# Kernel optimization log

Hardware: AMD Instinct MI355X
Metric: run time of the kernel (lower is better)

## Reference

```python
import jax, jax.numpy as jnp
import numpy as np

NUM_HEADS = 16
EPS = 1e-5
CHUNK = 128  # chunk length for the chunked recurrent-state scan


def _linear_attention(x, Wq, Wk, Wv, Wo, bo):
    B, T, E = x.shape
    H = NUM_HEADS
    d = E // H

    def proj(W):
        # nn.Linear(bias=False): y = x @ W.T ; split heads -> (B,H,T,d)
        return (x @ W.T).reshape(B, T, H, d).transpose(0, 2, 1, 3)

    phi_q = jax.nn.elu(proj(Wq)) + 1.0
    phi_k = jax.nn.elu(proj(Wk)) + 1.0
    V = proj(Wv)

    nC = T // CHUNK
    # (nC, B, H, C, d) so lax.scan iterates over chunks of time
    def to_chunks(a):
        return a.reshape(B, H, nC, CHUNK, d).transpose(2, 0, 1, 3, 4)

    qc, kc, vc = to_chunks(phi_q), to_chunks(phi_k), to_chunks(V)
    mask = jnp.tril(jnp.ones((CHUNK, CHUNK), x.dtype))  # causal incl. diagonal

    S0 = jnp.zeros((B, H, d, d), x.dtype)  # running sum of k v^T
    z0 = jnp.zeros((B, H, d), x.dtype)     # running sum of phi_k

    def step(carry, inp):
        S, z = carry
        q, k, v = inp  # (B,H,C,d)
        A = jnp.einsum('bhid,bhjd->bhij', q, k) * mask
        num = jnp.einsum('bhij,bhjd->bhid', A, v) + jnp.einsum('bhid,bhde->bhie', q, S)
        den = jnp.sum(A, axis=-1) + jnp.einsum('bhid,bhd->bhi', q, z) + EPS
        out = num / den[..., None]
        S = S + jnp.einsum('bhjd,bhje->bhde', k, v)
        z = z + jnp.sum(k, axis=2)
        return (S, z), out

    _, outs = jax.lax.scan(step, (S0, z0), (qc, kc, vc))  # (nC,B,H,C,d)
    out = outs.transpose(1, 2, 0, 3, 4).reshape(B, H, T, d)
    out = out.transpose(0, 2, 1, 3).reshape(B, T, E)
    # out_proj (dropout p=0 / eval -> identity)
    return out @ Wo.T + bo


def setup_inputs() -> dict:
    key = jax.random.key(0)
    ks = jax.random.split(key, 6)
    B, T, E = 2, 2048, 1024
    s = 1.0 / np.sqrt(E)
    return {
        'x': jax.random.normal(ks[0], (B, T, E), jnp.float32),
        'Wq': jax.random.normal(ks[1], (E, E), jnp.float32) * s,
        'Wk': jax.random.normal(ks[2], (E, E), jnp.float32) * s,
        'Wv': jax.random.normal(ks[3], (E, E), jnp.float32) * s,
        'Wo': jax.random.normal(ks[4], (E, E), jnp.float32) * s,
        'bo': jnp.zeros((E,), jnp.float32),
    }


def reference(x, Wq, Wk, Wv, Wo, bo):
    return _linear_attention(x, Wq, Wk, Wv, Wo, bo)
```

## Files before the change

### kernel.cpp

```cpp
#include <hip/hip_runtime.h>
#include <hip/hip_bf16.h>
#include <stdint.h>

typedef __attribute__((ext_vector_type(4)))  float  floatx4;
typedef __attribute__((ext_vector_type(8)))  short  short8;
typedef __attribute__((ext_vector_type(8)))  unsigned short ushortx8;
typedef __attribute__((ext_vector_type(4)))  unsigned short ushortx4;

#define B_  2
#define T_  2048
#define E_  1024
#define H_  16
#define D_  64
#define C_  128
#define NC_ 16
#define M_  4096
#define EPS_ 1e-5f

__device__ __forceinline__ unsigned short f2b(float f) {
    union { float f; unsigned int u; } v; v.f = f;
    unsigned int r = v.u + 0x7fffu + ((v.u >> 16) & 1u);
    return (unsigned short)(r >> 16);
}
__device__ __forceinline__ float b2f(unsigned short b) {
    union { unsigned int u; float f; } v; v.u = ((unsigned int)b) << 16;
    return v.f;
}

__device__ __forceinline__ int stage_seg(int i) { return (i & 3) ^ ((i >> 3) & 3); }
__device__ __forceinline__ int frag_slot(int lane) {
    int m = lane & 15, q = lane >> 4;
    return m * 4 + (q ^ ((m >> 1) & 3));
}

__global__ __launch_bounds__(256) void convert_all(const float* __restrict__ x,
                                                   const float* __restrict__ Wq,
                                                   const float* __restrict__ Wk,
                                                   const float* __restrict__ Wv,
                                                   const float* __restrict__ Wo,
                                                   unsigned short* __restrict__ dst) {
    int i = (blockIdx.x * 256 + threadIdx.x) * 4;
    const float* s; int off;
    if (i < M_ * E_) { s = x; off = i; }
    else {
        int j = i - M_ * E_;
        int which = j >> 20;
        s = (which == 0) ? Wq : (which == 1) ? Wk : (which == 2) ? Wv : Wo;
        off = j & ((1 << 20) - 1);
    }
    float4 f = *(const float4*)(s + off);
    ushortx4 o;
    o[0] = f2b(f.x); o[1] = f2b(f.y); o[2] = f2b(f.z); o[3] = f2b(f.w);
    *(ushortx4*)(dst + i) = o;
}

__global__ __launch_bounds__(512) void gemm_qkv(const unsigned short* __restrict__ A,
                                                const unsigned short* __restrict__ Bm,
                                                unsigned short* __restrict__ Cb) {
    const int N = 3 * E_, K = E_;
    __shared__ __align__(16) unsigned short smem[57344];
    unsigned short* at0 = smem;
    unsigned short* bt0 = smem + 16384;
    unsigned short* at1 = smem + 28672;
    unsigned short* bt1 = smem + 45056;
    int tid = threadIdx.x;
    int wave = tid >> 6, lane = tid & 63;
    int wr = wave >> 2, wc = wave & 3;
    int m = lane & 15, q = lane >> 4;
    int srow = lane >> 2, sseg = stage_seg(lane);
    int fs = frag_slot(lane);
    int row0 = blockIdx.y * 256, col0 = blockIdx.x * 192;
    floatx4 acc[8][3];
    for (int i = 0; i < 8; i++) for (int j = 0; j < 3; j++) acc[i][j] = floatx4{0.f, 0.f, 0.f, 0.f};

    auto stageA = [&](unsigned short* at, int k0) {
        for (int p = 0; p < 4; p++) {
            int t = p * 8 + wave;
            const unsigned short* ga = A + (size_t)(row0 + (t & 15) * 16 + srow) * K + k0 + (t >> 4) * 32 + sseg * 8;
            __builtin_amdgcn_global_load_lds((const __attribute__((address_space(1))) unsigned int*)ga,
                (__attribute__((address_space(3))) unsigned int*)(at + t * 512), 16, 0, 0);
        }
    };
    auto stageB = [&](unsigned short* bt, int k0) {
        for (int p = 0; p < 3; p++) {
            int u = p * 8 + wave;
            int kh = u / 12, rb = u - kh * 12;
            const unsigned short* gb = Bm + (size_t)(col0 + rb * 16 + srow) * K + k0 + kh * 32 + sseg * 8;
            __builtin_amdgcn_global_load_lds((const __attribute__((address_space(1))) unsigned int*)gb,
                (__attribute__((address_space(3))) unsigned int*)(bt + u * 512), 16, 0, 0);
        }
    };
    short8 af[8], bf[3];
    auto frags = [&](const unsigned short* at, const unsigned short* bt, int kh) {
        for (int mi = 0; mi < 8; mi++) af[mi] = *(const short8*)(at + (kh * 16 + wr * 8 + mi) * 512 + fs * 8);
        for (int ni = 0; ni < 3; ni++) bf[ni] = *(const short8*)(bt + (kh * 12 + wc * 3 + ni) * 512 + fs * 8);
    };
    auto mfma24 = [&]() {
        __builtin_amdgcn_s_setprio(1);
        for (int mi = 0; mi < 8; mi++)
            for (int ni = 0; ni < 3; ni++)
                acc[mi][ni] = __builtin_amdgcn_mfma_f32_16x16x32_bf16(af[mi], bf[ni], acc[mi][ni], 0, 0, 0);
        __builtin_amdgcn_s_setprio(0);
    };

    stageA(at0, 0); stageB(bt0, 0);
    for (int k0 = 0; k0 < K; k0 += 128) {
        stageA(at1, k0 + 64);
        asm volatile("s_waitcnt vmcnt(4)" ::: "memory");
        __builtin_amdgcn_s_barrier();
        frags(at0, bt0, 0);
        mfma24();
        frags(at0, bt0, 1);
        stageB(bt1, k0 + 64);
        mfma24();
        __builtin_amdgcn_s_barrier();
        if (k0 + 128 < K) {
            stageA(at0, k0 + 128);
            asm volatile("s_waitcnt vmcnt(4)" ::: "memory");
        } else {
            asm volatile("s_waitcnt vmcnt(0)" ::: "memory");
        }
        __builtin_amdgcn_s_barrier();
        frags(at1, bt1, 0);
        mfma24();
        frags(at1, bt1, 1);
        if (k0 + 128 < K) stageB(bt0, k0 + 128);
        mfma24();
        __builtin_amdgcn_s_barrier();
    }

    unsigned short* epi = smem + wave * 1792;
    for (int ch = 0; ch < 4; ch++) {
        if (ch) asm volatile("" ::: "memory");
        for (int mi2 = 0; mi2 < 2; mi2++) {
            int mi = ch * 2 + mi2;
            for (int ni = 0; ni < 3; ni++)
                for (int reg = 0; reg < 4; reg++) {
                    int lr = mi2 * 16 + q * 4 + reg;
                    int colw = col0 + wc * 48 + ni * 16 + m;
                    float v = acc[mi][ni][reg];
                    if (colw < 2 * E_) v = (v > 0.f) ? (v + 1.f) : __expf(v);
                    epi[lr * 56 + ni * 16 + m] = f2b(v);
                }
        }
        asm volatile("" ::: "memory");
        for (int slot = 0; slot < 3; slot++) {
            int s = slot * 64 + lane;
            int lr = s / 6, seg = s - lr * 6;
            const unsigned short* p = epi + lr * 56 + seg * 8;
            ushortx4 lo = *(const ushortx4*)(p);
            ushortx4 hi = *(const ushortx4*)(p + 4);
            ushortx8 val;
            for (int e = 0; e < 4; e++) { val[e] = lo[e]; val[e + 4] = hi[e]; }
            int row = row0 + wr * 128 + ch * 32 + lr;
            int col = col0 + wc * 48 + seg * 8;
            *(ushortx8*)(Cb + (size_t)row * N + col) = val;
        }
    }
}

__global__ __launch_bounds__(256) void gemm_out(const unsigned short* __restrict__ A,
                                                const unsigned short* __restrict__ Bm,
                                                const float* __restrict__ bias,
                                                float* __restrict__ Cf) {
    const int N = E_, K = E_;
    __shared__ __align__(16) unsigned short smem[24576];
    unsigned short* at0 = smem;
    unsigned short* bt0 = smem + 8192;
    unsigned short* at1 = smem + 12288;
    unsigned short* bt1 = smem + 20480;
    int tid = threadIdx.x;
    int wave = tid >> 6, lane = tid & 63;
    int wr = wave >> 1, wc = wave & 1;
    int m = lane & 15, q = lane >> 4;
    int srow = lane >> 2, sseg = stage_seg(lane);
    int fs = frag_slot(lane);
    int row0 = blockIdx.y * 128, col0 = blockIdx.x * 64;
    floatx4 acc[4][2];
    for (int i = 0; i < 4; i++) for (int j = 0; j < 2; j++) acc[i][j] = floatx4{0.f, 0.f, 0.f, 0.f};

    auto stageA = [&](unsigned short* at, int k0) {
        for (int p = 0; p < 4; p++) {
            int t = p * 4 + wave;
            const unsigned short* ga = A + (size_t)(row0 + (t & 7) * 16 + srow) * K + k0 + (t >> 3) * 32 + sseg * 8;
            __builtin_amdgcn_global_load_lds((const __attribute__((address_space(1))) unsigned int*)ga,
                (__attribute__((address_space(3))) unsigned int*)(at + t * 512), 16, 0, 0);
        }
    };
    auto stageB = [&](unsigned short* bt, int k0) {
        for (int p = 0; p < 2; p++) {
            int u = p * 4 + wave;
            const unsigned short* gb = Bm + (size_t)(col0 + (u & 3) * 16 + srow) * K + k0 + (u >> 2) * 32 + sseg * 8;
            __builtin_amdgcn_global_load_lds((const __attribute__((address_space(1))) unsigned int*)gb,
                (__attribute__((address_space(3))) unsigned int*)(bt + u * 512), 16, 0, 0);
        }
    };
    short8 af[4], bf[2];
    auto frags = [&](const unsigned short* at, const unsigned short* bt, int kh) {
        for (int mi = 0; mi < 4; mi++) af[mi] = *(const short8*)(at + (kh * 8 + wr * 4 + mi) * 512 + fs * 8);
        for (int ci = 0; ci < 2; ci++) bf[ci] = *(const short8*)(bt + (kh * 4 + wc * 2 + ci) * 512 + fs * 8);
    };
    auto mfma8 = [&]() {
        __builtin_amdgcn_s_setprio(1);
        for (int mi = 0; mi < 4; mi++)
            for (int ci = 0; ci < 2; ci++)
                acc[mi][ci] = __builtin_amdgcn_mfma_f32_16x16x32_bf16(af[mi], bf[ci], acc[mi][ci], 0, 0, 0);
        __builtin_amdgcn_s_setprio(0);
    };

    stageA(at0, 0); stageB(bt0, 0);
    for (int k0 = 0; k0 < K; k0 += 128) {
        stageA(at1, k0 + 64);
        asm volatile("s_waitcnt vmcnt(4)" ::: "memory");
        __builtin_amdgcn_s_barrier();
        frags(at0, bt0, 0);
        mfma8();
        frags(at0, bt0, 1);
        stageB(bt1, k0 + 64);
        mfma8();
        __builtin_amdgcn_s_barrier();
        if (k0 + 128 < K) {
            stageA(at0, k0 + 128);
            asm volatile("s_waitcnt vmcnt(4)" ::: "memory");
        } else {
            asm volatile("s_waitcnt vmcnt(0)" ::: "memory");
        }
        __builtin_amdgcn_s_barrier();
        frags(at1, bt1, 0);
        mfma8();
        frags(at1, bt1, 1);
        if (k0 + 128 < K) stageB(bt0, k0 + 128);
        mfma8();
        __builtin_amdgcn_s_barrier();
    }

    int qrow = q * 4;
    for (int ci = 0; ci < 2; ci++) {
        int col = col0 + wc * 32 + ci * 16 + m;
        float bv = bias[col];
        for (int mi = 0; mi < 4; mi++)
            for (int r2 = 0; r2 < 4; r2++) {
                int row = row0 + wr * 64 + mi * 16 + qrow + r2;
                Cf[(size_t)row * N + col] = acc[mi][ci][r2] + bv;
            }
    }
}

__global__ __launch_bounds__(256) void chunk_sums(const unsigned short* __restrict__ qkv,
                                                  float* __restrict__ Sc, float* __restrict__ zc) {
    int c = blockIdx.x, h = blockIdx.y, bb = blockIdx.z;
    __shared__ __align__(16) unsigned short Kt[64 * 132];
    __shared__ __align__(16) unsigned short Vt[80 * 132];
    int tid = threadIdx.x;
    int lane = tid & 63, w = tid >> 6;
    size_t rowb = (size_t)bb * T_ + (size_t)c * C_;
    int kcol = E_ + h * D_, vcol = 2 * E_ + h * D_;

    {
        int r4 = (tid >> 3) * 4;
        int seg = (tid & 7) * 8;
        ushortx8 kv[4], vv[4];
        for (int t = 0; t < 4; t++) {
            size_t g = (rowb + r4 + t) * 3072;
            kv[t] = *(const ushortx8*)(qkv + g + kcol + seg);
            vv[t] = *(const ushortx8*)(qkv + g + vcol + seg);
        }
        for (int e = 0; e < 8; e++) {
            ushortx4 ka, va;
            for (int t = 0; t < 4; t++) { ka[t] = kv[t][e]; va[t] = vv[t][e]; }
            *(ushortx4*)(Kt + (seg + e) * 132 + r4) = ka;
            *(ushortx4*)(Vt + (seg + e) * 132 + r4) = va;
        }
    }
    if (tid < 128) Vt[64 * 132 + tid] = 0x3f80;
    __syncthreads();

    floatx4 acc[5];
    for (int ni = 0; ni < 5; ni++) acc[ni] = floatx4{0.f, 0.f, 0.f, 0.f};
    int lm = lane & 15, lk = (lane >> 4) * 8;
    for (int k0 = 0; k0 < 128; k0 += 32) {
        short8 af = *(const short8*)(Kt + (w * 16 + lm) * 132 + k0 + lk);
        for (int ni = 0; ni < 5; ni++) {
            short8 bf = *(const short8*)(Vt + (ni * 16 + lm) * 132 + k0 + lk);
            acc[ni] = __builtin_amdgcn_mfma_f32_16x16x32_bf16(af, bf, acc[ni], 0, 0, 0);
        }
    }
    size_t base = ((size_t)(bb * H_ + h) * NC_ + c) * (size_t)(D_ * D_);
    int r0 = w * 16 + (lane >> 4) * 4;
    for (int ni = 0; ni < 4; ni++)
        for (int reg = 0; reg < 4; reg++)
            Sc[base + (size_t)(r0 + reg) * D_ + ni * 16 + lm] = acc[ni][reg];
    if (lm == 0) {
        size_t zb = ((size_t)(bb * H_ + h) * NC_ + c) * D_;
        for (int reg = 0; reg < 4; reg++) zc[zb + r0 + reg] = acc[4][reg];
    }
}

__global__ __launch_bounds__(256) void attn_kernel(const unsigned short* __restrict__ qkv,
                                                   const float* __restrict__ Sc,
                                                   const float* __restrict__ zc,
                                                   unsigned short* __restrict__ attn) {
    int c = blockIdx.x, h = blockIdx.y, bb = blockIdx.z;
    __shared__ __align__(16) unsigned short ks[128 * 68];
    __shared__ __align__(16) unsigned short vt[64 * 132];
    __shared__ __align__(16) unsigned short ovl[128 * 36];
    __shared__ float zsh[64];
    int tid = threadIdx.x;
    int lane = tid & 63, w = tid >> 6;
    int lm = lane & 15, lq = lane >> 4;
    size_t rowb = (size_t)bb * T_ + (size_t)c * C_;
    int qcol = h * D_, kcol = E_ + h * D_, vcol = 2 * E_ + h * D_;

    for (int s = 0; s < 4; s++) {
        int off = s * 256 + tid;
        int r = off >> 3, seg = (off & 7) * 8;
        ushortx8 k8 = *(const ushortx8*)(qkv + (rowb + r) * 3072 + kcol + seg);
        *(ushortx8*)(ks + r * 68 + seg) = k8;
    }
    {
        int r4 = (tid >> 3) * 4;
        int seg = (tid & 7) * 8;
        ushortx8 vv[4];
        for (int t = 0; t < 4; t++)
            vv[t] = *(const ushortx8*)(qkv + (rowb + r4 + t) * 3072 + vcol + seg);
        for (int e = 0; e < 8; e++) {
            ushortx4 va;
            for (int t = 0; t < 4; t++) va[t] = vv[t][e];
            *(ushortx4*)(vt + (seg + e) * 132 + r4) = va;
        }
    }
    {
        size_t scb = ((size_t)(bb * H_ + h) * NC_) * (size_t)(D_ * D_);
        int p = tid * 16;
        float a[16];
        for (int i = 0; i < 16; i++) a[i] = 0.f;
        for (int j = 0; j < c; j++) {
            const float* Sj = Sc + scb + (size_t)j * (D_ * D_) + p;
            for (int q = 0; q < 16; q += 4) {
                float4 f = *(const float4*)(Sj + q);
                a[q] += f.x; a[q + 1] += f.y; a[q + 2] += f.z; a[q + 3] += f.w;
            }
        }
        for (int i = 0; i < 16; i++) {
            int d = (p + i) >> 6, e = (p + i) & 63;
            ovl[e * 68 + d] = f2b(a[i]);
        }
    }
    if (tid < 64) {
        size_t zb = ((size_t)(bb * H_ + h) * NC_) * D_;
        float zr = 0.f;
        for (int j = 0; j < c; j++) zr += zc[zb + (size_t)j * D_ + tid];
        zsh[tid] = zr;
    }

    short8 aq[2][2];
    for (int mi = 0; mi < 2; mi++)
        for (int kk = 0; kk < 2; kk++)
            aq[mi][kk] = *(const short8*)(qkv + (rowb + w * 32 + mi * 16 + lm) * 3072 + qcol + kk * 32 + lq * 8);
    __syncthreads();

    floatx4 acc[2][4];
    for (int mi = 0; mi < 2; mi++) for (int ni = 0; ni < 4; ni++) acc[mi][ni] = floatx4{0.f, 0.f, 0.f, 0.f};
    for (int kk = 0; kk < 2; kk++)
        for (int ni = 0; ni < 4; ni++) {
            short8 bs = *(const short8*)(ovl + (ni * 16 + lm) * 68 + kk * 32 + lq * 8);
            for (int mi = 0; mi < 2; mi++)
                acc[mi][ni] = __builtin_amdgcn_mfma_f32_16x16x32_bf16(aq[mi][kk], bs, acc[mi][ni], 0, 0, 0);
        }
    float dsum[2][4];
    {
        float4 z4 = *(const float4*)(zsh + lm * 4);
        for (int mi = 0; mi < 2; mi++)
            for (int reg = 0; reg < 4; reg++) {
                int row = w * 32 + mi * 16 + lq * 4 + reg;
                ushortx4 q4 = *(const ushortx4*)(qkv + (rowb + row) * 3072 + qcol + lm * 4);
                dsum[mi][reg] = b2f(q4[0]) * z4.x + b2f(q4[1]) * z4.y + b2f(q4[2]) * z4.z + b2f(q4[3]) * z4.w;
            }
    }
    __syncthreads();

    for (int jt = 0; jt <= w; jt++) {
        floatx4 pa[2][2];
        for (int mi = 0; mi < 2; mi++) for (int ct = 0; ct < 2; ct++) pa[mi][ct] = floatx4{0.f, 0.f, 0.f, 0.f};
        for (int kk = 0; kk < 2; kk++)
            for (int ct = 0; ct < 2; ct++) {
                short8 bk = *(const short8*)(ks + (jt * 32 + ct * 16 + lm) * 68 + kk * 32 + lq * 8);
                for (int mi = 0; mi < 2; mi++)
                    pa[mi][ct] = __builtin_amdgcn_mfma_f32_16x16x32_bf16(aq[mi][kk], bk, pa[mi][ct], 0, 0, 0);
            }
        bool diag = (jt == w);
        for (int mi = 0; mi < 2; mi++)
            for (int ct = 0; ct < 2; ct++)
                for (int reg = 0; reg < 4; reg++) {
                    int il = mi * 16 + lq * 4 + reg;
                    int jl = ct * 16 + lm;
                    float v = pa[mi][ct][reg];
                    if (diag && jl > il) v = 0.f;
                    dsum[mi][reg] += v;
                    ovl[(w * 32 + il) * 36 + jl] = f2b(v);
                }
        short8 ap[2];
        for (int mi = 0; mi < 2; mi++)
            ap[mi] = *(const short8*)(ovl + (w * 32 + mi * 16 + lm) * 36 + lq * 8);
        for (int ni = 0; ni < 4; ni++) {
            short8 bv = *(const short8*)(vt + (ni * 16 + lm) * 132 + jt * 32 + lq * 8);
            for (int mi = 0; mi < 2; mi++)
                acc[mi][ni] = __builtin_amdgcn_mfma_f32_16x16x32_bf16(ap[mi], bv, acc[mi][ni], 0, 0, 0);
        }
    }

    for (int off = 1; off < 16; off <<= 1)
        for (int mi = 0; mi < 2; mi++)
            for (int reg = 0; reg < 4; reg++)
                dsum[mi][reg] += __shfl_xor(dsum[mi][reg], off);

    for (int mi = 0; mi < 2; mi++)
        for (int reg = 0; reg < 4; reg++) {
            float inv = 1.f / (dsum[mi][reg] + EPS_);
            int row = w * 32 + mi * 16 + lq * 4 + reg;
            for (int ni = 0; ni < 4; ni++)
                attn[(rowb + row) * E_ + h * D_ + ni * 16 + lm] = f2b(acc[mi][ni][reg] * inv);
        }
}

extern "C" void kernel_launch(void* const* d_in, const int* in_sizes, int n_in,
                              void* d_out, int out_size, void* d_ws, size_t ws_size,
                              hipStream_t stream) {
    const float* x  = (const float*)d_in[0];
    const float* Wq = (const float*)d_in[1];
    const float* Wk = (const float*)d_in[2];
    const float* Wv = (const float*)d_in[3];
    const float* Wo = (const float*)d_in[4];
    const float* bo = (const float*)d_in[5];
    float* out = (float*)d_out;

    const size_t MB = 1024 * 1024;
    uint8_t* ws = (uint8_t*)d_ws;
    unsigned short* xb    = (unsigned short*)(ws + 0);
    unsigned short* wb    = (unsigned short*)(ws + 8 * MB);
    unsigned short* wob   = wb + 3 * E_ * E_;
    unsigned short* qkvb  = (unsigned short*)(ws + 16 * MB);
    float* Sc = (float*)(ws + 40 * MB);
    float* zc = (float*)(ws + 48 * MB);
    unsigned short* attnb = xb;

    convert_all<<<(M_ * E_ + 4 * E_ * E_) / 1024, 256, 0, stream>>>(x, Wq, Wk, Wv, Wo, xb);

    gemm_qkv<<<dim3(16, 16), 512, 0, stream>>>(xb, wb, qkvb);
    chunk_sums<<<dim3(NC_, H_, B_), 256, 0, stream>>>(qkvb, Sc, zc);
    attn_kernel<<<dim3(NC_, H_, B_), 256, 0, stream>>>(qkvb, Sc, zc, attnb);
    gemm_out<<<dim3(16, 32), 256, 0, stream>>>(attnb, wob, bo, out);
}
```

Baseline: 157.0 us.

## Balance causal intra-chunk work across waves with paired 16-row blocks

Each wave now handles two 16-row query blocks (w and 7-w) instead of one contiguous 32-row block, so the triangular causal work in the attention kernel is spread evenly across the four waves. The inner loop is restructured to compute 16x16 score tiles and run the PV MFMA once per pair of key tiles, zero-padding the odd tail. This removes the imbalance where wave 3 did four times the work of wave 0. In exchange it adds more small MFMA sequences and some extra LDS traffic per tile.

```diff
diff --git a/kernel.cpp b/kernel.cpp
--- a/kernel.cpp
+++ b/kernel.cpp
@@ -310,6 +310,7 @@
     int lm = lane & 15, lq = lane >> 4;
     size_t rowb = (size_t)bb * T_ + (size_t)c * C_;
     int qcol = h * D_, kcol = E_ + h * D_, vcol = 2 * E_ + h * D_;
+    int rb[2] = { w, 7 - w };
 
     for (int s = 0; s < 4; s++) {
         int off = s * 256 + tid;
@@ -354,72 +355,74 @@
     }
 
     short8 aq[2][2];
-    for (int mi = 0; mi < 2; mi++)
+    for (int b = 0; b < 2; b++)
         for (int kk = 0; kk < 2; kk++)
-            aq[mi][kk] = *(const short8*)(qkv + (rowb + w * 32 + mi * 16 + lm) * 3072 + qcol + kk * 32 + lq * 8);
+            aq[b][kk] = *(const short8*)(qkv + (rowb + rb[b] * 16 + lm) * 3072 + qcol + kk * 32 + lq * 8);
     __syncthreads();
 
     floatx4 acc[2][4];
-    for (int mi = 0; mi < 2; mi++) for (int ni = 0; ni < 4; ni++) acc[mi][ni] = floatx4{0.f, 0.f, 0.f, 0.f};
+    for (int b = 0; b < 2; b++) for (int ni = 0; ni < 4; ni++) acc[b][ni] = floatx4{0.f, 0.f, 0.f, 0.f};
     for (int kk = 0; kk < 2; kk++)
         for (int ni = 0; ni < 4; ni++) {
             short8 bs = *(const short8*)(ovl + (ni * 16 + lm) * 68 + kk * 32 + lq * 8);
-            for (int mi = 0; mi < 2; mi++)
-                acc[mi][ni] = __builtin_amdgcn_mfma_f32_16x16x32_bf16(aq[mi][kk], bs, acc[mi][ni], 0, 0, 0);
+            for (int b = 0; b < 2; b++)
+                acc[b][ni] = __builtin_amdgcn_mfma_f32_16x16x32_bf16(aq[b][kk], bs, acc[b][ni], 0, 0, 0);
         }
     float dsum[2][4];
     {
         float4 z4 = *(const float4*)(zsh + lm * 4);
-        for (int mi = 0; mi < 2; mi++)
+        for (int b = 0; b < 2; b++)
             for (int reg = 0; reg < 4; reg++) {
-                int row = w * 32 + mi * 16 + lq * 4 + reg;
+                int row = rb[b] * 16 + lq * 4 + reg;
                 ushortx4 q4 = *(const ushortx4*)(qkv + (rowb + row) * 3072 + qcol + lm * 4);
-                dsum[mi][reg] = b2f(q4[0]) * z4.x + b2f(q4[1]) * z4.y + b2f(q4[2]) * z4.z + b2f(q4[3]) * z4.w;
+                dsum[b][reg] = b2f(q4[0]) * z4.x + b2f(q4[1]) * z4.y + b2f(q4[2]) * z4.z + b2f(q4[3]) * z4.w;
             }
     }
     __syncthreads();
 
-    for (int jt = 0; jt <= w; jt++) {
-        floatx4 pa[2][2];
-        for (int mi = 0; mi < 2; mi++) for (int ct = 0; ct < 2; ct++) pa[mi][ct] = floatx4{0.f, 0.f, 0.f, 0.f};
-        for (int kk = 0; kk < 2; kk++)
-            for (int ct = 0; ct < 2; ct++) {
-                short8 bk = *(const short8*)(ks + (jt * 32 + ct * 16 + lm) * 68 + kk * 32 + lq * 8);
-                for (int mi = 0; mi < 2; mi++)
-                    pa[mi][ct] = __builtin_amdgcn_mfma_f32_16x16x32_bf16(aq[mi][kk], bk, pa[mi][ct], 0, 0, 0);
-            }
-        bool diag = (jt == w);
-        for (int mi = 0; mi < 2; mi++)
-            for (int ct = 0; ct < 2; ct++)
-                for (int reg = 0; reg < 4; reg++) {
-                    int il = mi * 16 + lq * 4 + reg;
-                    int jl = ct * 16 + lm;
-                    float v = pa[mi][ct][reg];
-                    if (diag && jl > il) v = 0.f;
-                    dsum[mi][reg] += v;
-                    ovl[(w * 32 + il) * 36 + jl] = f2b(v);
+    for (int b = 0; b < 2; b++) {
+        int R = rb[b];
+        int prow = R * 16;
+        for (int jt = 0; jt <= R; jt++) {
+            floatx4 pa = floatx4{0.f, 0.f, 0.f, 0.f};
+            for (int kk = 0; kk < 2; kk++) {
+                short8 bk = *(const short8*)(ks + (jt * 16 + lm) * 68 + kk * 32 + lq * 8);
+                pa = __builtin_amdgcn_mfma_f32_16x16x32_bf16(aq[b][kk], bk, pa, 0, 0, 0);
+            }
+            bool diag = (jt == R);
+            for (int reg = 0; reg < 4; reg++) {
+                int il = lq * 4 + reg;
+                float v = pa[reg];
+                if (diag && lm > il) v = 0.f;
+                dsum[b][reg] += v;
+                ovl[(prow + il) * 36 + (jt & 1) * 16 + lm] = f2b(v);
+            }
+            if ((jt & 1) || jt == R) {
+                if (!(jt & 1)) {
+                    for (int reg = 0; reg < 4; reg++)
+                        ovl[(prow + lq * 4 + reg) * 36 + 16 + lm] = 0;
                 }
-        short8 ap[2];
-        for (int mi = 0; mi < 2; mi++)
-            ap[mi] = *(const short8*)(ovl + (w * 32 + mi * 16 + lm) * 36 + lq * 8);
-        for (int ni = 0; ni < 4; ni++) {
-            short8 bv = *(const short8*)(vt + (ni * 16 + lm) * 132 + jt * 32 + lq * 8);
-            for (int mi = 0; mi < 2; mi++)
-                acc[mi][ni] = __builtin_amdgcn_mfma_f32_16x16x32_bf16(ap[mi], bv, acc[mi][ni], 0, 0, 0);
+                int pair = jt >> 1;
+                short8 ap = *(const short8*)(ovl + (prow + lm) * 36 + lq * 8);
+                for (int ni = 0; ni < 4; ni++) {
+                    short8 bv = *(const short8*)(vt + (ni * 16 + lm) * 132 + pair * 32 + lq * 8);
+                    acc[b][ni] = __builtin_amdgcn_mfma_f32_16x16x32_bf16(ap, bv, acc[b][ni], 0, 0, 0);
+                }
+            }
         }
     }
 
     for (int off = 1; off < 16; off <<= 1)
-        for (int mi = 0; mi < 2; mi++)
+        for (int b = 0; b < 2; b++)
             for (int reg = 0; reg < 4; reg++)
-                dsum[mi][reg] += __shfl_xor(dsum[mi][reg], off);
-
-    for (int mi = 0; mi < 2; mi++)
+                dsum[b][reg] += __shfl_xor(dsum[b][reg], off);
+
+    for (int b = 0; b < 2; b++)
         for (int reg = 0; reg < 4; reg++) {
-            float inv = 1.f / (dsum[mi][reg] + EPS_);
-            int row = w * 32 + mi * 16 + lq * 4 + reg;
+            float inv = 1.f / (dsum[b][reg] + EPS_);
+            int row = rb[b] * 16 + lq * 4 + reg;
             for (int ni = 0; ni < 4; ni++)
-                attn[(rowb + row) * E_ + h * D_ + ni * 16 + lm] = f2b(acc[mi][ni][reg] * inv);
+                attn[(rowb + row) * E_ + h * D_ + ni * 16 + lm] = f2b(acc[b][ni][reg] * inv);
         }
 }
 
```

New measurement: 156.8 us. Within noise of the previous version (-0.1%).
